# Kernel optimization log

Measured on AMD Instinct MI355X. Metric: run time of the kernel, lower is better.

The kernel has to match this reference:

```python
import jax, jax.numpy as jnp
import numpy as np

N = 256        # nagents
HID = 256      # hid_size
OBS = 128      # obs_size
GAT_HID = 128  # gat_hid_size
H1 = 4         # gat_num_heads (first processor)
H2 = 1         # gat_num_heads_out (second processor)
NACT = 10      # single action head
NEG = 0.2      # leaky relu negative slope


def _lin(k, fan_in, fan_out, s=0.05):
    kw, kb = jax.random.split(k)
    return (jax.random.normal(kw, (fan_in, fan_out), jnp.float32) * s,
            jax.random.normal(kb, (fan_out,), jnp.float32) * s)


def setup_inputs() -> dict:
    key = jax.random.key(0)
    ks = jax.random.split(key, 32)
    p = {}
    p['obs'] = jax.random.normal(ks[0], (1, N, OBS), jnp.float32)
    p['hidden_state'] = jax.random.normal(ks[1], (N, HID), jnp.float32)
    p['cell_state'] = jax.random.normal(ks[2], (N, HID), jnp.float32)
    p['w_obs'], p['b_obs'] = _lin(ks[3], OBS, HID)
    p['w_ih'], p['b_ih'] = _lin(ks[4], HID, 4 * HID)   # LSTMCell input->gates (i,f,g,o)
    p['w_hh'], p['b_hh'] = _lin(ks[5], HID, 4 * HID)
    p['w_me'], p['b_me'] = _lin(ks[6], HID, HID)        # message encoder
    p['w_md'], p['b_md'] = _lin(ks[7], HID, HID)        # message decoder
    # sub_scheduler_mlp1: 2*HID -> HID//2 -> HID//8 -> 2
    p['s1_w1'], p['s1_b1'] = _lin(ks[8], 2 * HID, HID // 2)
    p['s1_w2'], p['s1_b2'] = _lin(ks[9], HID // 2, HID // 8)
    p['s1_w3'], p['s1_b3'] = _lin(ks[10], HID // 8, 2)
    # sub_scheduler_mlp2 (learn_second_graph)
    p['s2_w1'], p['s2_b1'] = _lin(ks[11], 2 * HID, HID // 2)
    p['s2_w2'], p['s2_b2'] = _lin(ks[12], HID // 2, HID // 8)
    p['s2_w3'], p['s2_b3'] = _lin(ks[13], HID // 8, 2)
    # GAT1: HID -> H1*GAT_HID (concat heads)
    p['g1_w'] = jax.random.normal(ks[14], (HID, H1 * GAT_HID), jnp.float32) * 0.05
    p['g1_ai'] = jax.random.normal(ks[15], (H1, GAT_HID), jnp.float32) * 0.05
    p['g1_aj'] = jax.random.normal(ks[16], (H1, GAT_HID), jnp.float32) * 0.05
    p['g1_b'] = jax.random.normal(ks[17], (H1 * GAT_HID,), jnp.float32) * 0.05
    # GAT2: H1*GAT_HID -> HID (average over heads)
    p['g2_w'] = jax.random.normal(ks[18], (H1 * GAT_HID, H2 * HID), jnp.float32) * 0.05
    p['g2_ai'] = jax.random.normal(ks[19], (H2, HID), jnp.float32) * 0.05
    p['g2_aj'] = jax.random.normal(ks[20], (H2, HID), jnp.float32) * 0.05
    p['g2_b'] = jax.random.normal(ks[21], (HID,), jnp.float32) * 0.05
    p['w_v'], p['b_v'] = _lin(ks[22], 2 * HID, 1)
    p['w_a'], p['b_a'] = _lin(ks[23], 2 * HID, NACT)
    return p


def _sub_scheduler(h, w1, b1, w2, b2, w3, b3, mask, key):
    # pairwise concat: pair[i,j] = [h_i, h_j]  -> [n, n, 2*hid]
    n, d = h.shape
    pair = jnp.concatenate([jnp.broadcast_to(h[:, None, :], (n, n, d)),
                            jnp.broadcast_to(h[None, :, :], (n, n, d))], axis=-1)
    z = jax.nn.relu(pair @ w1 + b1)
    z = jax.nn.relu(z @ w2 + b2)
    logits = z @ w3 + b3                                # [n, n, 2]
    # gumbel-softmax (tau=1, hard=True, straight-through)
    u = jax.random.uniform(key, logits.shape, minval=1e-10, maxval=1.0)
    gumbel = -jnp.log(-jnp.log(u))
    y = jax.nn.softmax(logits + gumbel, axis=-1)
    y_hard = jax.nn.one_hot(jnp.argmax(y, axis=-1), 2, dtype=y.dtype)
    y = y_hard + y - jax.lax.stop_gradient(y)
    adj = y[..., 1] * mask * mask.T                     # mask [n,1]
    return adj


def _gat(x, adj, W, ai, aj, b, average):
    # dense-adjacency multi-head GAT, self_loop_type=1 (force self loops)
    n = x.shape[0]
    heads, of = ai.shape
    h = (x @ W).reshape(n, heads, of)                   # [n, heads, out]
    eye = jnp.eye(n, dtype=x.dtype)
    adj = adj * (1.0 - eye) + eye
    ci = jnp.einsum('nhf,hf->nh', h, ai)
    cj = jnp.einsum('nhf,hf->nh', h, aj)
    e = jax.nn.leaky_relu(ci[:, None, :] + cj[None, :, :], NEG)   # [n, n, heads]
    att = jnp.where(adj[:, :, None] > 0, e, jnp.float32(-9e15))
    att = jax.nn.softmax(att, axis=1)
    att = att * adj[:, :, None]
    out = jnp.einsum('ijh,jhf->ihf', att, h)            # aggregate over neighbors j
    out = out.mean(axis=1) if average else out.reshape(n, heads * of)
    return out + b


def reference(obs, hidden_state, cell_state, w_obs, b_obs, w_ih, b_ih, w_hh, b_hh,
              w_me, b_me, w_md, b_md,
              s1_w1, s1_b1, s1_w2, s1_b2, s1_w3, s1_b3,
              s2_w1, s2_b1, s2_w2, s2_b2, s2_w3, s2_b3,
              g1_w, g1_ai, g1_aj, g1_b, g2_w, g2_ai, g2_aj, g2_b,
              w_v, b_v, w_a, b_a):
    x = (obs @ w_obs + b_obs)[0]                        # [n, hid]
    # LSTMCell, torch gate order (i, f, g, o)
    gates = x @ w_ih + b_ih + hidden_state @ w_hh + b_hh
    i, f, g, o = jnp.split(gates, 4, axis=-1)
    c_new = jax.nn.sigmoid(f) * cell_state + jax.nn.sigmoid(i) * jnp.tanh(g)
    h_new = jax.nn.sigmoid(o) * jnp.tanh(c_new)
    mask = jnp.ones((N, 1), jnp.float32)                # all agents alive
    comm = (h_new @ w_me + b_me) * mask
    comm_ori = comm
    adj1 = _sub_scheduler(comm, s1_w1, s1_b1, s1_w2, s1_b2, s1_w3, s1_b3,
                          mask, jax.random.key(1))
    comm = jax.nn.elu(_gat(comm, adj1, g1_w, g1_ai, g1_aj, g1_b, average=False))
    adj2 = _sub_scheduler(comm_ori, s2_w1, s2_b1, s2_w2, s2_b2, s2_w3, s2_b3,
                          mask, jax.random.key(2))
    comm = _gat(comm, adj2, g2_w, g2_ai, g2_aj, g2_b, average=True)
    comm = (comm * mask) @ w_md + b_md
    value = jnp.concatenate([h_new, comm], axis=-1) @ w_v + b_v      # [n, 1]
    hc = jnp.concatenate([h_new.reshape(1, N, HID), comm.reshape(1, N, HID)], axis=-1)
    action_out = jax.nn.log_softmax(hc @ w_a + b_a, axis=-1)         # [1, n, nact]
    return action_out, value, h_new, c_new
```

## Files before the change

kernel.cpp:

```cpp
#include <hip/hip_runtime.h>
#include <stdint.h>
#include <math.h>

#define NA 256

typedef __attribute__((ext_vector_type(4))) float f32x4;
typedef __attribute__((ext_vector_type(8))) short bfrag;
typedef __attribute__((ext_vector_type(4))) float cfrag;

__device__ __forceinline__ uint32_t rotl32_(uint32_t v, int d) {
    return (v << d) | (v >> (32 - d));
}

__device__ uint32_t jax_random_bits(uint32_t key_lo, uint32_t flat) {
    uint32_t a, b;
    bool first;
    if (flat < 65536u) { a = flat; b = flat + 65536u; first = true; }
    else               { a = flat - 65536u; b = flat; first = false; }
    uint32_t ks0 = 0u, ks1 = key_lo, ks2 = 0u ^ key_lo ^ 0x1BD11BDAu;
    uint32_t x0 = a + ks0, x1 = b + ks1;
    const int r0[4] = {13, 15, 26, 6};
    const int r1[4] = {17, 29, 16, 24};
#define TF_R4(RS) { for (int rr = 0; rr < 4; ++rr) { x0 += x1; x1 = rotl32_(x1, RS[rr]); x1 ^= x0; } }
    TF_R4(r0); x0 += ks1; x1 += ks2 + 1u;
    TF_R4(r1); x0 += ks2; x1 += ks0 + 2u;
    TF_R4(r0); x0 += ks0; x1 += ks1 + 3u;
    TF_R4(r1); x0 += ks1; x1 += ks2 + 4u;
    TF_R4(r0); x0 += ks2; x1 += ks0 + 5u;
#undef TF_R4
    return first ? x0 : x1;
}

__device__ float jax_gumbel(uint32_t key_lo, uint32_t flat) {
    uint32_t bits = jax_random_bits(key_lo, flat);
    uint32_t v = (bits >> 9) | 0x3F800000u;
    float u = __uint_as_float(v) - 1.0f;
    u = u + 1e-10f;
    u = fmaxf(1e-10f, u);
    return -logf(-logf(u));
}

__device__ __forceinline__ uint32_t f2bf(float f) {
    uint32_t u = __float_as_uint(f);
    return (u + 0x7FFFu + ((u >> 16) & 1u)) >> 16;
}

__global__ __launch_bounds__(256) void k_lstm(
        const float* __restrict__ obs, const float* __restrict__ hs,
        const float* __restrict__ cs,
        const float* __restrict__ w_obs, const float* __restrict__ b_obs,
        const float* __restrict__ w_ih, const float* __restrict__ b_ih,
        const float* __restrict__ w_hh, const float* __restrict__ b_hh,
        float* __restrict__ h_out, float* __restrict__ c_out) {
    __shared__ float o_l[8][128];
    __shared__ float h_l[8][256];
    __shared__ float x_l[8][256];
    __shared__ float red[8192];
    int r0 = blockIdx.x * 8, c0 = blockIdx.y * 32, t = threadIdx.x;
    ((f32x4*)o_l)[t] = ((const f32x4*)(obs + r0 * 128))[t];
    ((f32x4*)h_l)[t] = ((const f32x4*)(hs + r0 * 256))[t];
    ((f32x4*)h_l)[t + 256] = ((const f32x4*)(hs + r0 * 256))[t + 256];
    __syncthreads();
    {
        int ks = t >> 6, q = t & 63;
        f32x4 acc[8];
#pragma unroll
        for (int r = 0; r < 8; ++r) acc[r] = (f32x4){0.f, 0.f, 0.f, 0.f};
#pragma unroll
        for (int k = ks * 32; k < ks * 32 + 32; ++k) {
            f32x4 w = *(const f32x4*)(w_obs + k * 256 + q * 4);
#pragma unroll
            for (int r = 0; r < 8; ++r) {
                float xv = o_l[r][k];
                acc[r].x += xv * w.x; acc[r].y += xv * w.y;
                acc[r].z += xv * w.z; acc[r].w += xv * w.w;
            }
        }
#pragma unroll
        for (int r = 0; r < 8; ++r)
            *(f32x4*)&red[(ks * 8 + r) * 256 + q * 4] = acc[r];
    }
    __syncthreads();
    {
#pragma unroll
        for (int rep = 0; rep < 8; ++rep) {
            int o = t + rep * 256;
            int r = o >> 8, c = o & 255;
            float s = b_obs[c];
#pragma unroll
            for (int k2 = 0; k2 < 4; ++k2) s += red[(k2 * 8 + r) * 256 + c];
            x_l[r][c] = s;
        }
    }
    __syncthreads();
    {
        int ks = t >> 5, cg = t & 31;
        int g = cg >> 3, qd = cg & 7;
        int col = g * 256 + c0 + qd * 4;
        const float* W = (ks < 4) ? w_ih : w_hh;
        const float* xl = (ks < 4) ? &x_l[0][0] : &h_l[0][0];
        int kb = (ks & 3) * 64;
        f32x4 acc[8];
#pragma unroll
        for (int r = 0; r < 8; ++r) acc[r] = (f32x4){0.f, 0.f, 0.f, 0.f};
#pragma unroll
        for (int kk = 0; kk < 64; ++kk) {
            int k = kb + kk;
            f32x4 w = *(const f32x4*)(W + k * 1024 + col);
#pragma unroll
            for (int r = 0; r < 8; ++r) {
                float xv = xl[r * 256 + k];
                acc[r].x += xv * w.x; acc[r].y += xv * w.y;
                acc[r].z += xv * w.z; acc[r].w += xv * w.w;
            }
        }
        __syncthreads();
#pragma unroll
        for (int r = 0; r < 8; ++r)
            *(f32x4*)&red[(ks * 8 + r) * 128 + cg * 4] = acc[r];
    }
    __syncthreads();
    {
        int r = t >> 5, hc = t & 31;
        int gc = c0 + hc;
        float gate[4];
#pragma unroll
        for (int g = 0; g < 4; ++g) {
            float s = b_ih[g * 256 + gc] + b_hh[g * 256 + gc];
#pragma unroll
            for (int ks = 0; ks < 8; ++ks) s += red[(ks * 8 + r) * 128 + g * 32 + hc];
            gate[g] = s;
        }
        float ig = 1.f / (1.f + expf(-gate[0]));
        float fg = 1.f / (1.f + expf(-gate[1]));
        float gg = tanhf(gate[2]);
        float og = 1.f / (1.f + expf(-gate[3]));
        float cn = fg * cs[(r0 + r) * 256 + gc] + ig * gg;
        float hn = og * tanhf(cn);
        h_out[(r0 + r) * 256 + gc] = hn;
        c_out[(r0 + r) * 256 + gc] = cn;
    }
}

template<int K>
__device__ __forceinline__ void gemm_core(const float* __restrict__ X, int xs, int r0,
                                          const float* __restrict__ W, int ws,
                                          const float* __restrict__ bias,
                                          float* __restrict__ Y, int ys, int t,
                                          float* xr, float* red) {
    constexpr int KQ = K / 4;
#pragma unroll
    for (int q = t; q < 2 * K; q += 256) {
        int r = q / KQ, c = q % KQ;
        ((f32x4*)xr)[r * KQ + c] = ((const f32x4*)(X + (r0 + r) * xs))[c];
    }
    __syncthreads();
    constexpr int KP = K / 16;
    int qd = t & 15, ks = t >> 4;
    f32x4 acc[8];
#pragma unroll
    for (int r = 0; r < 8; ++r) acc[r] = (f32x4){0.f, 0.f, 0.f, 0.f};
#pragma unroll
    for (int k = ks * KP; k < ks * KP + KP; ++k) {
        f32x4 w = *(const f32x4*)(W + k * ws + qd * 4);
#pragma unroll
        for (int r = 0; r < 8; ++r) {
            float xv = xr[r * K + k];
            acc[r].x += xv * w.x; acc[r].y += xv * w.y;
            acc[r].z += xv * w.z; acc[r].w += xv * w.w;
        }
    }
#pragma unroll
    for (int r = 0; r < 8; ++r)
        *(f32x4*)&red[(ks * 8 + r) * 64 + qd * 4] = acc[r];
    __syncthreads();
#pragma unroll
    for (int rep = 0; rep < 2; ++rep) {
        int o = t + rep * 256;
        int r = o >> 6, c = o & 63;
        float s = bias ? bias[c] : 0.f;
#pragma unroll
        for (int ks2 = 0; ks2 < 16; ++ks2) s += red[(ks2 * 8 + r) * 64 + c];
        Y[(r0 + r) * ys + c] = s;
    }
}

template<int K>
__global__ __launch_bounds__(256) void k_gemm(const float* __restrict__ X, int xs,
                                              const float* __restrict__ W, int ws,
                                              const float* __restrict__ bias,
                                              float* __restrict__ Y, int ys) {
    __shared__ float xr[8 * K];
    __shared__ float red[16 * 8 * 64];
    int cb = blockIdx.y * 64;
    gemm_core<K>(X, xs, blockIdx.x * 8, W + cb, ws, bias ? bias + cb : nullptr,
                 Y + cb, ys, threadIdx.x, xr, red);
}

__global__ __launch_bounds__(256) void k_mgemm(const float* __restrict__ comm,
        const float* __restrict__ g1_w,
        const float* __restrict__ s1w1, const float* __restrict__ s1b1,
        const float* __restrict__ s2w1, const float* __restrict__ s2b1,
        float* __restrict__ h1, float* __restrict__ A1, float* __restrict__ B1,
        float* __restrict__ A2, float* __restrict__ B2) {
    __shared__ float xr[8 * 256];
    __shared__ float red[16 * 8 * 64];
    int y = blockIdx.y;
    const float* W; int ws; const float* bias; float* Y; int ys;
    if (y < 8) {
        W = g1_w + y * 64; ws = 512; bias = nullptr; Y = h1 + y * 64; ys = 512;
    } else {
        int idx = y - 8;
        int sel = idx >> 2, part = (idx >> 1) & 1, half = idx & 1;
        W = (sel ? s2w1 : s1w1) + part * (256 * 128) + half * 64; ws = 128;
        bias = part ? nullptr : ((sel ? s2b1 : s1b1) + half * 64);
        float* tgt = sel ? (part ? B2 : A2) : (part ? B1 : A1);
        Y = tgt + half * 64; ys = 128;
    }
    gemm_core<256>(comm, 256, blockIdx.x * 8, W, ws, bias, Y, ys, threadIdx.x, xr, red);
}

__global__ __launch_bounds__(256) void k_sched(
        const float* __restrict__ A1, const float* __restrict__ B1,
        const float* __restrict__ s1w2, const float* __restrict__ s1b2,
        const float* __restrict__ s1w3, const float* __restrict__ s1b3,
        const float* __restrict__ A2, const float* __restrict__ B2,
        const float* __restrict__ s2w2, const float* __restrict__ s2b2,
        const float* __restrict__ s2w3, const float* __restrict__ s2b3,
        float* __restrict__ adj1, float* __restrict__ adj2) {
    __shared__ __align__(16) char z1z2[65536];
    __shared__ __align__(16) char w2l[8192];
    __shared__ float a_l[128];
    __shared__ float b2_l[32], w3_l[64], b3_l[2];
    int i = blockIdx.x, t = threadIdx.x, s = blockIdx.y;
    const float* A  = s ? A2 : A1;
    const float* B  = s ? B2 : B1;
    const float* w2 = s ? s2w2 : s1w2;
    const float* b2 = s ? s2b2 : s1b2;
    const float* w3 = s ? s2w3 : s1w3;
    const float* b3 = s ? s2b3 : s1b3;
    float* adj = s ? adj2 : adj1;
    uint32_t key_lo = (uint32_t)(s + 1);

    if (t < 32) ((f32x4*)a_l)[t] = ((const f32x4*)(A + i * 128))[t];
    if (t < 32) b2_l[t] = b2[t];
    if (t < 64) w3_l[t] = w3[t];
    if (t < 2)  b3_l[t] = b3[t];
    {
        int c = t & 31, kq = t >> 5;
        uint32_t* dst = (uint32_t*)w2l;
#pragma unroll
        for (int e = 0; e < 8; ++e) {
            int k = kq * 16 + e * 2;
            uint32_t word = f2bf(w2[k * 32 + c]) | (f2bf(w2[(k + 1) * 32 + c]) << 16);
            int byte = (c * 256 + k * 2) ^ ((c & 7) << 4);
            dst[byte >> 2] = word;
        }
    }
    __syncthreads();
#pragma unroll
    for (int rep = 0; rep < 4; ++rep) {
        int j = (t >> 2) + rep * 64;
        int kq = t & 3;
        const f32x4* bp = (const f32x4*)(B + j * 128 + kq * 32);
        uint32_t words[16];
#pragma unroll
        for (int q = 0; q < 8; ++q) {
            f32x4 bv = bp[q];
            int k = kq * 32 + q * 4;
            float z0 = fmaxf(a_l[k] + bv.x, 0.f);
            float z1v = fmaxf(a_l[k + 1] + bv.y, 0.f);
            float z2v = fmaxf(a_l[k + 2] + bv.z, 0.f);
            float z3v = fmaxf(a_l[k + 3] + bv.w, 0.f);
            words[q * 2]     = f2bf(z0) | (f2bf(z1v) << 16);
            words[q * 2 + 1] = f2bf(z2v) | (f2bf(z3v) << 16);
        }
#pragma unroll
        for (int w4 = 0; w4 < 4; ++w4) {
            int byte = (j * 256 + kq * 64 + w4 * 16) ^ ((j & 7) << 4);
            *(uint4*)(z1z2 + byte) = make_uint4(words[w4 * 4], words[w4 * 4 + 1],
                                                words[w4 * 4 + 2], words[w4 * 4 + 3]);
        }
    }
    __syncthreads();
    int w = t >> 6, l = t & 63;
    bfrag bf[2][4];
#pragma unroll
    for (int ct = 0; ct < 2; ++ct)
#pragma unroll
        for (int ks = 0; ks < 4; ++ks) {
            int col = ct * 16 + (l & 15);
            int k = ks * 32 + (l >> 4) * 8;
            int byte = (col * 256 + k * 2) ^ ((col & 7) << 4);
            bf[ct][ks] = *(bfrag*)(w2l + byte);
        }
    cfrag acc[4][2];
    cfrag zz = {0.f, 0.f, 0.f, 0.f};
#pragma unroll
    for (int rt = 0; rt < 4; ++rt) { acc[rt][0] = zz; acc[rt][1] = zz; }
#pragma unroll
    for (int rt = 0; rt < 4; ++rt) {
        int j = (w * 4 + rt) * 16 + (l & 15);
#pragma unroll
        for (int ks = 0; ks < 4; ++ks) {
            int byte = (j * 256 + (ks * 32 + (l >> 4) * 8) * 2) ^ ((j & 7) << 4);
            bfrag af = *(bfrag*)(z1z2 + byte);
            acc[rt][0] = __builtin_amdgcn_mfma_f32_16x16x32_bf16(af, bf[0][ks], acc[rt][0], 0, 0, 0);
            acc[rt][1] = __builtin_amdgcn_mfma_f32_16x16x32_bf16(af, bf[1][ks], acc[rt][1], 0, 0, 0);
        }
    }
    __syncthreads();
    float* z2 = (float*)z1z2;
#pragma unroll
    for (int rt = 0; rt < 4; ++rt)
#pragma unroll
        for (int ct = 0; ct < 2; ++ct)
#pragma unroll
            for (int r = 0; r < 4; ++r) {
                int j = (w * 4 + rt) * 16 + (l >> 4) * 4 + r;
                int c = ct * 16 + (l & 15);
                z2[j * 36 + c] = acc[rt][ct][r];
            }
    __syncthreads();
    {
        int j = t;
        float p0 = 0.f, p1 = 0.f;
#pragma unroll
        for (int c = 0; c < 32; ++c) {
            float zv = fmaxf(z2[j * 36 + c] + b2_l[c], 0.f);
            p0 += zv * w3_l[2 * c];
            p1 += zv * w3_l[2 * c + 1];
        }
        float l0 = p0 + b3_l[0], l1 = p1 + b3_l[1];
        uint32_t flat = (uint32_t)(i * 256 + j) * 2u;
        float g0 = jax_gumbel(key_lo, flat);
        float g1 = jax_gumbel(key_lo, flat + 1u);
        adj[i * 256 + j] = (l1 + g1 > l0 + g0) ? 1.0f : 0.0f;
    }
}

__global__ void k_attc(const float* __restrict__ H, const float* __restrict__ ai,
                       const float* __restrict__ aj, float* __restrict__ ci,
                       float* __restrict__ cj, int heads, int F) {
    int n = blockIdx.x, lane = threadIdx.x;
    for (int h = 0; h < heads; ++h) {
        float pi = 0.f, pj = 0.f;
        for (int f = lane; f < F; f += 64) {
            float v = H[n * heads * F + h * F + f];
            pi += v * ai[h * F + f];
            pj += v * aj[h * F + f];
        }
        for (int off = 32; off; off >>= 1) {
            pi += __shfl_xor(pi, off);
            pj += __shfl_xor(pj, off);
        }
        if (lane == 0) { ci[n * heads + h] = pi; cj[n * heads + h] = pj; }
    }
}

__global__ __launch_bounds__(256) void k_gat1(const float* __restrict__ H,
        const float* __restrict__ adj, const float* __restrict__ ci,
        const float* __restrict__ cj, const float* __restrict__ bias,
        float* __restrict__ out) {
    __shared__ float att[2][4][256];
    __shared__ float red[4][2][256];
    int i0 = blockIdx.x * 2, cb = blockIdx.y * 256, t = threadIdx.x;
#pragma unroll
    for (int r = 0; r < 2; ++r) {
        int i = i0 + r;
        float adjv = (t == i) ? 1.f : adj[i * 256 + t];
#pragma unroll
        for (int h = 0; h < 4; ++h) {
            float e = ci[i * 4 + h] + cj[t * 4 + h];
            e = e >= 0.f ? e : 0.2f * e;
            att[r][h][t] = adjv > 0.f ? e : -INFINITY;
        }
    }
    __syncthreads();
    {
        int wv = t >> 6, lane = t & 63;
        for (int p = wv; p < 8; p += 4) {
            int r = p >> 2, h = p & 3;
            float* ar = att[r][h];
            float m = -INFINITY;
            for (int j = lane; j < 256; j += 64) m = fmaxf(m, ar[j]);
            for (int off = 32; off; off >>= 1) m = fmaxf(m, __shfl_xor(m, off));
            float vals[4], sm = 0.f;
#pragma unroll
            for (int q = 0; q < 4; ++q) {
                float v = expf(ar[lane + 64 * q] - m);
                vals[q] = v; sm += v;
            }
            for (int off = 32; off; off >>= 1) sm += __shfl_xor(sm, off);
            float inv = 1.f / sm;
#pragma unroll
            for (int q = 0; q < 4; ++q) ar[lane + 64 * q] = vals[q] * inv;
        }
    }
    __syncthreads();
    {
        int q = t & 63, js = t >> 6;
        int c = cb + q * 4;
        int h = c >> 7;
        f32x4 a0 = {0.f, 0.f, 0.f, 0.f}, a1 = a0;
        const float* ar0 = att[0][h];
        const float* ar1 = att[1][h];
#pragma unroll
        for (int j = js * 64; j < js * 64 + 64; ++j) {
            f32x4 hv = *(const f32x4*)(H + j * 512 + c);
            float v0 = ar0[j], v1 = ar1[j];
            a0.x += v0 * hv.x; a0.y += v0 * hv.y; a0.z += v0 * hv.z; a0.w += v0 * hv.w;
            a1.x += v1 * hv.x; a1.y += v1 * hv.y; a1.z += v1 * hv.z; a1.w += v1 * hv.w;
        }
        *(f32x4*)&red[js][0][q * 4] = a0;
        *(f32x4*)&red[js][1][q * 4] = a1;
    }
    __syncthreads();
#pragma unroll
    for (int rep = 0; rep < 2; ++rep) {
        int o = t + rep * 256;
        int r = o >> 8, c = o & 255;
        float s = red[0][r][c] + red[1][r][c] + red[2][r][c] + red[3][r][c] + bias[cb + c];
        out[(i0 + r) * 512 + cb + c] = s > 0.f ? s : expm1f(s);
    }
}

__global__ __launch_bounds__(256) void k_final(const float* __restrict__ H,
        const float* __restrict__ adj, const float* __restrict__ ci,
        const float* __restrict__ cj, const float* __restrict__ g2_b,
        const float* __restrict__ w_md, const float* __restrict__ b_md,
        const float* __restrict__ h_new,
        const float* __restrict__ w_v, const float* __restrict__ b_v,
        const float* __restrict__ w_a, const float* __restrict__ b_a,
        float* __restrict__ value, float* __restrict__ action) {
    __shared__ float att[256];
    __shared__ float buf[4][256];
    __shared__ float out2[256];
    __shared__ float comm3[256];
    __shared__ float hrow[256];
    __shared__ float hred[4][16];
    __shared__ float vred[4];
    int i = blockIdx.x, t = threadIdx.x;
    hrow[t] = h_new[i * 256 + t];
    {
        float adjv = (t == i) ? 1.f : adj[i * 256 + t];
        float e = ci[i] + cj[t];
        e = e >= 0.f ? e : 0.2f * e;
        att[t] = adjv > 0.f ? e : -INFINITY;
    }
    __syncthreads();
    {
        int lane = t & 63;
        float m = -INFINITY;
        for (int j = lane; j < 256; j += 64) m = fmaxf(m, att[j]);
        for (int off = 32; off; off >>= 1) m = fmaxf(m, __shfl_xor(m, off));
        float sm = 0.f;
        for (int j = lane; j < 256; j += 64) sm += expf(att[j] - m);
        for (int off = 32; off; off >>= 1) sm += __shfl_xor(sm, off);
        float inv = 1.f / sm;
        float myval = expf(att[t] - m) * inv;
        __syncthreads();
        att[t] = myval;
    }
    __syncthreads();
    {
        int q = t & 63, js = t >> 6;
        f32x4 acc = {0.f, 0.f, 0.f, 0.f};
#pragma unroll
        for (int j = js * 64; j < js * 64 + 64; ++j) {
            f32x4 hv = *(const f32x4*)(H + j * 256 + q * 4);
            float av = att[j];
            acc.x += av * hv.x; acc.y += av * hv.y; acc.z += av * hv.z; acc.w += av * hv.w;
        }
        *(f32x4*)&buf[js][q * 4] = acc;
    }
    __syncthreads();
    out2[t] = buf[0][t] + buf[1][t] + buf[2][t] + buf[3][t] + g2_b[t];
    __syncthreads();
    {
        int q = t & 63, ks = t >> 6;
        f32x4 acc = {0.f, 0.f, 0.f, 0.f};
#pragma unroll
        for (int k = ks * 64; k < ks * 64 + 64; ++k) {
            f32x4 wv = *(const f32x4*)(w_md + k * 256 + q * 4);
            float xv = out2[k];
            acc.x += xv * wv.x; acc.y += xv * wv.y; acc.z += xv * wv.z; acc.w += xv * wv.w;
        }
        *(f32x4*)&buf[ks][q * 4] = acc;
    }
    __syncthreads();
    comm3[t] = buf[0][t] + buf[1][t] + buf[2][t] + buf[3][t] + b_md[t];
    __syncthreads();
    int w = t >> 6, l = t & 63;
    {
        float p = hrow[t] * w_v[t] + comm3[t] * w_v[256 + t];
        for (int off = 32; off; off >>= 1) p += __shfl_xor(p, off);
        if (l == 0) vred[w] = p;
    }
    {
        int o = l & 15;
        int kseg = w * 4 + (l >> 4);
        float acc = 0.f;
        if (o < 10) {
#pragma unroll
            for (int kk = 0; kk < 32; ++kk) {
                int k = kseg * 32 + kk;
                float x = (kseg < 8) ? hrow[k] : comm3[k - 256];
                acc += x * w_a[k * 10 + o];
            }
        }
        acc += __shfl_xor(acc, 16);
        acc += __shfl_xor(acc, 32);
        if (l < 16) hred[w][l] = acc;
    }
    __syncthreads();
    if (t < 16) {
        int o = t;
        float logit = (o < 10)
            ? hred[0][o] + hred[1][o] + hred[2][o] + hred[3][o] + b_a[o]
            : -INFINITY;
        float m = logit;
        for (int off = 8; off; off >>= 1) m = fmaxf(m, __shfl_xor(m, off));
        float ex = (o < 10) ? expf(logit - m) : 0.f;
        float sm = ex;
        for (int off = 8; off; off >>= 1) sm += __shfl_xor(sm, off);
        if (o < 10) action[i * 10 + o] = logit - m - logf(sm);
        if (o == 0) value[i] = vred[0] + vred[1] + vred[2] + vred[3] + b_v[0];
    }
}

extern "C" void kernel_launch(void* const* d_in, const int* in_sizes, int n_in,
                              void* d_out, int out_size, void* d_ws, size_t ws_size,
                              hipStream_t stream) {
    const float* obs   = (const float*)d_in[0];
    const float* hs    = (const float*)d_in[1];
    const float* cs    = (const float*)d_in[2];
    const float* w_obs = (const float*)d_in[3];
    const float* b_obs = (const float*)d_in[4];
    const float* w_ih  = (const float*)d_in[5];
    const float* b_ih  = (const float*)d_in[6];
    const float* w_hh  = (const float*)d_in[7];
    const float* b_hh  = (const float*)d_in[8];
    const float* w_me  = (const float*)d_in[9];
    const float* b_me  = (const float*)d_in[10];
    const float* w_md  = (const float*)d_in[11];
    const float* b_md  = (const float*)d_in[12];
    const float* s1_w1 = (const float*)d_in[13];
    const float* s1_b1 = (const float*)d_in[14];
    const float* s1_w2 = (const float*)d_in[15];
    const float* s1_b2 = (const float*)d_in[16];
    const float* s1_w3 = (const float*)d_in[17];
    const float* s1_b3 = (const float*)d_in[18];
    const float* s2_w1 = (const float*)d_in[19];
    const float* s2_b1 = (const float*)d_in[20];
    const float* s2_w2 = (const float*)d_in[21];
    const float* s2_b2 = (const float*)d_in[22];
    const float* s2_w3 = (const float*)d_in[23];
    const float* s2_b3 = (const float*)d_in[24];
    const float* g1_w  = (const float*)d_in[25];
    const float* g1_ai = (const float*)d_in[26];
    const float* g1_aj = (const float*)d_in[27];
    const float* g1_b  = (const float*)d_in[28];
    const float* g2_w  = (const float*)d_in[29];
    const float* g2_ai = (const float*)d_in[30];
    const float* g2_aj = (const float*)d_in[31];
    const float* g2_b  = (const float*)d_in[32];
    const float* w_v   = (const float*)d_in[33];
    const float* b_v   = (const float*)d_in[34];
    const float* w_a   = (const float*)d_in[35];
    const float* b_a   = (const float*)d_in[36];

    float* out = (float*)d_out;
    float* action = out;
    float* value  = out + 2560;
    float* h_new  = out + 2816;
    float* c_new  = out + 68352;

    float* ws = (float*)d_ws;
    float* comm  = ws;
    float* A1    = ws + 65536;
    float* B1    = ws + 98304;
    float* A2    = ws + 131072;
    float* B2    = ws + 163840;
    float* adj1  = ws + 196608;
    float* adj2  = ws + 262144;
    float* h1    = ws + 327680;
    float* ci1   = ws + 458752;
    float* cj1   = ws + 459776;
    float* comm2 = ws + 460800;
    float* h2    = ws + 591872;
    float* ci2   = ws + 657408;
    float* cj2   = ws + 657664;

    k_lstm<<<dim3(32, 8), 256, 0, stream>>>(obs, hs, cs, w_obs, b_obs,
                                            w_ih, b_ih, w_hh, b_hh, h_new, c_new);
    k_gemm<256><<<dim3(32, 4), 256, 0, stream>>>(h_new, 256, w_me, 256, b_me, comm, 256);
    k_mgemm<<<dim3(32, 16), 256, 0, stream>>>(comm, g1_w, s1_w1, s1_b1, s2_w1, s2_b1,
                                              h1, A1, B1, A2, B2);
    k_sched<<<dim3(256, 2), 256, 0, stream>>>(A1, B1, s1_w2, s1_b2, s1_w3, s1_b3,
                                              A2, B2, s2_w2, s2_b2, s2_w3, s2_b3,
                                              adj1, adj2);
    k_attc<<<NA, 64, 0, stream>>>(h1, g1_ai, g1_aj, ci1, cj1, 4, 128);
    k_gat1<<<dim3(128, 2), 256, 0, stream>>>(h1, adj1, ci1, cj1, g1_b, comm2);
    k_gemm<512><<<dim3(32, 4), 256, 0, stream>>>(comm2, 512, g2_w, 256, nullptr, h2, 256);
    k_attc<<<NA, 64, 0, stream>>>(h2, g2_ai, g2_aj, ci2, cj2, 1, 256);
    k_final<<<NA, 256, 0, stream>>>(h2, adj2, ci2, cj2, g2_b, w_md, b_md, h_new,
                                    w_v, b_v, w_a, b_a, value, action);
}
```

Baseline: 73.71 us.

## Fuse all stages into one cooperative persistent kernel with grid syncs

```diff
diff --git a/kernel.cpp b/kernel.cpp
--- a/kernel.cpp
+++ b/kernel.cpp
@@ -1,12 +1,15 @@
 #include <hip/hip_runtime.h>
+#include <hip/hip_cooperative_groups.h>
 #include <stdint.h>
 #include <math.h>
 
-#define NA 256
+namespace cg = cooperative_groups;
 
 typedef __attribute__((ext_vector_type(4))) float f32x4;
 typedef __attribute__((ext_vector_type(8))) short bfrag;
 typedef __attribute__((ext_vector_type(4))) float cfrag;
+
+#define SM_BYTES 53248
 
 __device__ __forceinline__ uint32_t rotl32_(uint32_t v, int d) {
     return (v << d) | (v >> (32 - d));
@@ -45,21 +48,27 @@
     return (u + 0x7FFFu + ((u >> 16) & 1u)) >> 16;
 }
 
-__global__ __launch_bounds__(256) void k_lstm(
-        const float* __restrict__ obs, const float* __restrict__ hs,
-        const float* __restrict__ cs,
-        const float* __restrict__ w_obs, const float* __restrict__ b_obs,
-        const float* __restrict__ w_ih, const float* __restrict__ b_ih,
-        const float* __restrict__ w_hh, const float* __restrict__ b_hh,
-        float* __restrict__ h_out, float* __restrict__ c_out) {
-    __shared__ float o_l[8][128];
-    __shared__ float h_l[8][256];
-    __shared__ float x_l[8][256];
-    __shared__ float red[8192];
-    int r0 = blockIdx.x * 8, c0 = blockIdx.y * 32, t = threadIdx.x;
-    ((f32x4*)o_l)[t] = ((const f32x4*)(obs + r0 * 128))[t];
-    ((f32x4*)h_l)[t] = ((const f32x4*)(hs + r0 * 256))[t];
-    ((f32x4*)h_l)[t + 256] = ((const f32x4*)(hs + r0 * 256))[t + 256];
+struct KParams {
+    const float *obs, *hs, *cs, *w_obs, *b_obs, *w_ih, *b_ih, *w_hh, *b_hh;
+    const float *w_me, *b_me, *w_md, *b_md;
+    const float *s1w1, *s1b1, *s1w2, *s1b2, *s1w3, *s1b3;
+    const float *s2w1, *s2b1, *s2w2, *s2b2, *s2w3, *s2b3;
+    const float *g1w, *g1ai, *g1aj, *g1b, *g2w, *g2ai, *g2aj, *g2b;
+    const float *wv, *bv, *wa, *ba;
+    float *h_new, *c_new, *value, *action;
+    float *comm, *A1, *B1, *A2, *B2, *adj1, *adj2, *h1, *ci1, *cj1;
+    float *comm2, *h2, *ci2, *cj2;
+};
+
+__device__ __forceinline__ void lstm_stage(const KParams& p, char* SM, int b, int t) {
+    float* o_l = (float*)SM;
+    float* h_l = (float*)(SM + 4096);
+    float* x_l = (float*)(SM + 12288);
+    float* red = (float*)(SM + 20480);
+    int r0 = (b & 31) * 8, c0 = (b >> 5) * 32;
+    ((f32x4*)o_l)[t] = ((const f32x4*)(p.obs + r0 * 128))[t];
+    ((f32x4*)h_l)[t] = ((const f32x4*)(p.hs + r0 * 256))[t];
+    ((f32x4*)h_l)[t + 256] = ((const f32x4*)(p.hs + r0 * 256))[t + 256];
     __syncthreads();
     {
         int ks = t >> 6, q = t & 63;
@@ -68,10 +77,10 @@
         for (int r = 0; r < 8; ++r) acc[r] = (f32x4){0.f, 0.f, 0.f, 0.f};
 #pragma unroll
         for (int k = ks * 32; k < ks * 32 + 32; ++k) {
-            f32x4 w = *(const f32x4*)(w_obs + k * 256 + q * 4);
+            f32x4 w = *(const f32x4*)(p.w_obs + k * 256 + q * 4);
 #pragma unroll
             for (int r = 0; r < 8; ++r) {
-                float xv = o_l[r][k];
+                float xv = o_l[r * 128 + k];
                 acc[r].x += xv * w.x; acc[r].y += xv * w.y;
                 acc[r].z += xv * w.z; acc[r].w += xv * w.w;
             }
@@ -81,24 +90,22 @@
             *(f32x4*)&red[(ks * 8 + r) * 256 + q * 4] = acc[r];
     }
     __syncthreads();
-    {
-#pragma unroll
-        for (int rep = 0; rep < 8; ++rep) {
-            int o = t + rep * 256;
-            int r = o >> 8, c = o & 255;
-            float s = b_obs[c];
-#pragma unroll
-            for (int k2 = 0; k2 < 4; ++k2) s += red[(k2 * 8 + r) * 256 + c];
-            x_l[r][c] = s;
-        }
-    }
-    __syncthreads();
-    {
-        int ks = t >> 5, cg = t & 31;
-        int g = cg >> 3, qd = cg & 7;
-        int col = g * 256 + c0 + qd * 4;
-        const float* W = (ks < 4) ? w_ih : w_hh;
-        const float* xl = (ks < 4) ? &x_l[0][0] : &h_l[0][0];
+#pragma unroll
+    for (int rep = 0; rep < 8; ++rep) {
+        int o = t + rep * 256;
+        int r = o >> 8, c = o & 255;
+        float s = p.b_obs[c];
+#pragma unroll
+        for (int k2 = 0; k2 < 4; ++k2) s += red[(k2 * 8 + r) * 256 + c];
+        x_l[r * 256 + c] = s;
+    }
+    __syncthreads();
+    {
+        int ks = t >> 5, cg2 = t & 31;
+        int g2 = cg2 >> 3, qd = cg2 & 7;
+        int col = g2 * 256 + c0 + qd * 4;
+        const float* W = (ks < 4) ? p.w_ih : p.w_hh;
+        const float* xl = (ks < 4) ? x_l : h_l;
         int kb = (ks & 3) * 64;
         f32x4 acc[8];
 #pragma unroll
@@ -117,7 +124,7 @@
         __syncthreads();
 #pragma unroll
         for (int r = 0; r < 8; ++r)
-            *(f32x4*)&red[(ks * 8 + r) * 128 + cg * 4] = acc[r];
+            *(f32x4*)&red[(ks * 8 + r) * 128 + cg2 * 4] = acc[r];
     }
     __syncthreads();
     {
@@ -125,26 +132,26 @@
         int gc = c0 + hc;
         float gate[4];
 #pragma unroll
-        for (int g = 0; g < 4; ++g) {
-            float s = b_ih[g * 256 + gc] + b_hh[g * 256 + gc];
-#pragma unroll
-            for (int ks = 0; ks < 8; ++ks) s += red[(ks * 8 + r) * 128 + g * 32 + hc];
-            gate[g] = s;
+        for (int g2 = 0; g2 < 4; ++g2) {
+            float s = p.b_ih[g2 * 256 + gc] + p.b_hh[g2 * 256 + gc];
+#pragma unroll
+            for (int ks = 0; ks < 8; ++ks) s += red[(ks * 8 + r) * 128 + g2 * 32 + hc];
+            gate[g2] = s;
         }
         float ig = 1.f / (1.f + expf(-gate[0]));
         float fg = 1.f / (1.f + expf(-gate[1]));
         float gg = tanhf(gate[2]);
         float og = 1.f / (1.f + expf(-gate[3]));
-        float cn = fg * cs[(r0 + r) * 256 + gc] + ig * gg;
+        float cn = fg * p.cs[(r0 + r) * 256 + gc] + ig * gg;
         float hn = og * tanhf(cn);
-        h_out[(r0 + r) * 256 + gc] = hn;
-        c_out[(r0 + r) * 256 + gc] = cn;
+        p.h_new[(r0 + r) * 256 + gc] = hn;
+        p.c_new[(r0 + r) * 256 + gc] = cn;
     }
 }
 
 template<int K>
 __device__ __forceinline__ void gemm_core(const float* __restrict__ X, int xs, int r0,
-                                          const float* __restrict__ W, int ws,
+                                          const float* __restrict__ W, int wsb,
                                           const float* __restrict__ bias,
                                           float* __restrict__ Y, int ys, int t,
                                           float* xr, float* red) {
@@ -162,7 +169,7 @@
     for (int r = 0; r < 8; ++r) acc[r] = (f32x4){0.f, 0.f, 0.f, 0.f};
 #pragma unroll
     for (int k = ks * KP; k < ks * KP + KP; ++k) {
-        f32x4 w = *(const f32x4*)(W + k * ws + qd * 4);
+        f32x4 w = *(const f32x4*)(W + k * wsb + qd * 4);
 #pragma unroll
         for (int r = 0; r < 8; ++r) {
             float xv = xr[r * K + k];
@@ -185,61 +192,52 @@
     }
 }
 
-template<int K>
-__global__ __launch_bounds__(256) void k_gemm(const float* __restrict__ X, int xs,
-                                              const float* __restrict__ W, int ws,
-                                              const float* __restrict__ bias,
-                                              float* __restrict__ Y, int ys) {
-    __shared__ float xr[8 * K];
-    __shared__ float red[16 * 8 * 64];
-    int cb = blockIdx.y * 64;
-    gemm_core<K>(X, xs, blockIdx.x * 8, W + cb, ws, bias ? bias + cb : nullptr,
-                 Y + cb, ys, threadIdx.x, xr, red);
-}
-
-__global__ __launch_bounds__(256) void k_mgemm(const float* __restrict__ comm,
-        const float* __restrict__ g1_w,
-        const float* __restrict__ s1w1, const float* __restrict__ s1b1,
-        const float* __restrict__ s2w1, const float* __restrict__ s2b1,
-        float* __restrict__ h1, float* __restrict__ A1, float* __restrict__ B1,
-        float* __restrict__ A2, float* __restrict__ B2) {
-    __shared__ float xr[8 * 256];
-    __shared__ float red[16 * 8 * 64];
-    int y = blockIdx.y;
-    const float* W; int ws; const float* bias; float* Y; int ys;
-    if (y < 8) {
-        W = g1_w + y * 64; ws = 512; bias = nullptr; Y = h1 + y * 64; ys = 512;
-    } else {
-        int idx = y - 8;
-        int sel = idx >> 2, part = (idx >> 1) & 1, half = idx & 1;
-        W = (sel ? s2w1 : s1w1) + part * (256 * 128) + half * 64; ws = 128;
-        bias = part ? nullptr : ((sel ? s2b1 : s1b1) + half * 64);
-        float* tgt = sel ? (part ? B2 : A2) : (part ? B1 : A1);
-        Y = tgt + half * 64; ys = 128;
-    }
-    gemm_core<256>(comm, 256, blockIdx.x * 8, W, ws, bias, Y, ys, threadIdx.x, xr, red);
-}
-
-__global__ __launch_bounds__(256) void k_sched(
-        const float* __restrict__ A1, const float* __restrict__ B1,
-        const float* __restrict__ s1w2, const float* __restrict__ s1b2,
-        const float* __restrict__ s1w3, const float* __restrict__ s1b3,
-        const float* __restrict__ A2, const float* __restrict__ B2,
-        const float* __restrict__ s2w2, const float* __restrict__ s2b2,
-        const float* __restrict__ s2w3, const float* __restrict__ s2b3,
-        float* __restrict__ adj1, float* __restrict__ adj2) {
-    __shared__ __align__(16) char z1z2[65536];
-    __shared__ __align__(16) char w2l[8192];
-    __shared__ float a_l[128];
-    __shared__ float b2_l[32], w3_l[64], b3_l[2];
-    int i = blockIdx.x, t = threadIdx.x, s = blockIdx.y;
-    const float* A  = s ? A2 : A1;
-    const float* B  = s ? B2 : B1;
-    const float* w2 = s ? s2w2 : s1w2;
-    const float* b2 = s ? s2b2 : s1b2;
-    const float* w3 = s ? s2w3 : s1w3;
-    const float* b3 = s ? s2b3 : s1b3;
-    float* adj = s ? adj2 : adj1;
+__device__ __forceinline__ void comm_stage(const KParams& p, char* SM, int b, int t) {
+    if (b >= 128) return;
+    float* xr = (float*)SM;
+    float* red = (float*)(SM + 16384);
+    int cb = (b >> 5) * 64;
+    gemm_core<256>(p.h_new, 256, (b & 31) * 8, p.w_me + cb, 256, p.b_me + cb,
+                   p.comm + cb, 256, t, xr, red);
+}
+
+__device__ __forceinline__ void mgemm_stage(const KParams& p, char* SM, int b, int t) {
+    float* xr = (float*)SM;
+    float* red = (float*)(SM + 16384);
+    int bx = b & 31;
+#pragma unroll
+    for (int pass = 0; pass < 2; ++pass) {
+        int y = (b >> 5) + pass * 8;
+        const float* W; int wsb; const float* bias; float* Y; int ys;
+        if (y < 8) {
+            W = p.g1w + y * 64; wsb = 512; bias = nullptr; Y = p.h1 + y * 64; ys = 512;
+        } else {
+            int idx = y - 8;
+            int sel = idx >> 2, part = (idx >> 1) & 1, half = idx & 1;
+            W = (sel ? p.s2w1 : p.s1w1) + part * (256 * 128) + half * 64; wsb = 128;
+            bias = part ? nullptr : ((sel ? p.s2b1 : p.s1b1) + half * 64);
+            float* tgt = sel ? (part ? p.B2 : p.A2) : (part ? p.B1 : p.A1);
+            Y = tgt + half * 64; ys = 128;
+        }
+        gemm_core<256>(p.comm, 256, bx * 8, W, wsb, bias, Y, ys, t, xr, red);
+        __syncthreads();
+    }
+}
+
+__device__ __forceinline__ void sched_body(const KParams& p, char* SM, int i, int s, int t) {
+    char* z1z2 = SM;
+    char* w2l  = SM + 32768;
+    float* a_l  = (float*)(SM + 40960);
+    float* b2_l = (float*)(SM + 41472);
+    float* w3_l = (float*)(SM + 41600);
+    float* b3_l = (float*)(SM + 41856);
+    const float* A  = s ? p.A2 : p.A1;
+    const float* B  = s ? p.B2 : p.B1;
+    const float* w2 = s ? p.s2w2 : p.s1w2;
+    const float* b2 = s ? p.s2b2 : p.s1b2;
+    const float* w3 = s ? p.s2w3 : p.s1w3;
+    const float* b3 = s ? p.s2b3 : p.s1b3;
+    float* adj = s ? p.adj2 : p.adj1;
     uint32_t key_lo = (uint32_t)(s + 1);
 
     if (t < 32) ((f32x4*)a_l)[t] = ((const f32x4*)(A + i * 128))[t];
@@ -258,31 +256,6 @@
         }
     }
     __syncthreads();
-#pragma unroll
-    for (int rep = 0; rep < 4; ++rep) {
-        int j = (t >> 2) + rep * 64;
-        int kq = t & 3;
-        const f32x4* bp = (const f32x4*)(B + j * 128 + kq * 32);
-        uint32_t words[16];
-#pragma unroll
-        for (int q = 0; q < 8; ++q) {
-            f32x4 bv = bp[q];
-            int k = kq * 32 + q * 4;
-            float z0 = fmaxf(a_l[k] + bv.x, 0.f);
-            float z1v = fmaxf(a_l[k + 1] + bv.y, 0.f);
-            float z2v = fmaxf(a_l[k + 2] + bv.z, 0.f);
-            float z3v = fmaxf(a_l[k + 3] + bv.w, 0.f);
-            words[q * 2]     = f2bf(z0) | (f2bf(z1v) << 16);
-            words[q * 2 + 1] = f2bf(z2v) | (f2bf(z3v) << 16);
-        }
-#pragma unroll
-        for (int w4 = 0; w4 < 4; ++w4) {
-            int byte = (j * 256 + kq * 64 + w4 * 16) ^ ((j & 7) << 4);
-            *(uint4*)(z1z2 + byte) = make_uint4(words[w4 * 4], words[w4 * 4 + 1],
-                                                words[w4 * 4 + 2], words[w4 * 4 + 3]);
-        }
-    }
-    __syncthreads();
     int w = t >> 6, l = t & 63;
     bfrag bf[2][4];
 #pragma unroll
@@ -294,94 +267,124 @@
             int byte = (col * 256 + k * 2) ^ ((col & 7) << 4);
             bf[ct][ks] = *(bfrag*)(w2l + byte);
         }
-    cfrag acc[4][2];
-    cfrag zz = {0.f, 0.f, 0.f, 0.f};
-#pragma unroll
-    for (int rt = 0; rt < 4; ++rt) { acc[rt][0] = zz; acc[rt][1] = zz; }
-#pragma unroll
-    for (int rt = 0; rt < 4; ++rt) {
-        int j = (w * 4 + rt) * 16 + (l & 15);
-#pragma unroll
-        for (int ks = 0; ks < 4; ++ks) {
-            int byte = (j * 256 + (ks * 32 + (l >> 4) * 8) * 2) ^ ((j & 7) << 4);
-            bfrag af = *(bfrag*)(z1z2 + byte);
-            acc[rt][0] = __builtin_amdgcn_mfma_f32_16x16x32_bf16(af, bf[0][ks], acc[rt][0], 0, 0, 0);
-            acc[rt][1] = __builtin_amdgcn_mfma_f32_16x16x32_bf16(af, bf[1][ks], acc[rt][1], 0, 0, 0);
-        }
-    }
-    __syncthreads();
-    float* z2 = (float*)z1z2;
-#pragma unroll
-    for (int rt = 0; rt < 4; ++rt)
-#pragma unroll
-        for (int ct = 0; ct < 2; ++ct)
-#pragma unroll
-            for (int r = 0; r < 4; ++r) {
-                int j = (w * 4 + rt) * 16 + (l >> 4) * 4 + r;
-                int c = ct * 16 + (l & 15);
-                z2[j * 36 + c] = acc[rt][ct][r];
-            }
-    __syncthreads();
-    {
-        int j = t;
-        float p0 = 0.f, p1 = 0.f;
-#pragma unroll
-        for (int c = 0; c < 32; ++c) {
-            float zv = fmaxf(z2[j * 36 + c] + b2_l[c], 0.f);
-            p0 += zv * w3_l[2 * c];
-            p1 += zv * w3_l[2 * c + 1];
-        }
-        float l0 = p0 + b3_l[0], l1 = p1 + b3_l[1];
-        uint32_t flat = (uint32_t)(i * 256 + j) * 2u;
-        float g0 = jax_gumbel(key_lo, flat);
-        float g1 = jax_gumbel(key_lo, flat + 1u);
-        adj[i * 256 + j] = (l1 + g1 > l0 + g0) ? 1.0f : 0.0f;
-    }
-}
-
-__global__ void k_attc(const float* __restrict__ H, const float* __restrict__ ai,
-                       const float* __restrict__ aj, float* __restrict__ ci,
-                       float* __restrict__ cj, int heads, int F) {
-    int n = blockIdx.x, lane = threadIdx.x;
-    for (int h = 0; h < heads; ++h) {
-        float pi = 0.f, pj = 0.f;
-        for (int f = lane; f < F; f += 64) {
-            float v = H[n * heads * F + h * F + f];
-            pi += v * ai[h * F + f];
-            pj += v * aj[h * F + f];
-        }
-        for (int off = 32; off; off >>= 1) {
-            pi += __shfl_xor(pi, off);
-            pj += __shfl_xor(pj, off);
-        }
-        if (lane == 0) { ci[n * heads + h] = pi; cj[n * heads + h] = pj; }
-    }
-}
-
-__global__ __launch_bounds__(256) void k_gat1(const float* __restrict__ H,
-        const float* __restrict__ adj, const float* __restrict__ ci,
-        const float* __restrict__ cj, const float* __restrict__ bias,
-        float* __restrict__ out) {
-    __shared__ float att[2][4][256];
-    __shared__ float red[4][2][256];
-    int i0 = blockIdx.x * 2, cb = blockIdx.y * 256, t = threadIdx.x;
+#pragma unroll
+    for (int jh = 0; jh < 2; ++jh) {
+        int jb = jh * 128;
+#pragma unroll
+        for (int rep = 0; rep < 2; ++rep) {
+            int jl = (t >> 2) + rep * 64;
+            int kq = t & 3;
+            const f32x4* bp = (const f32x4*)(B + (jb + jl) * 128 + kq * 32);
+            uint32_t words[16];
+#pragma unroll
+            for (int q = 0; q < 8; ++q) {
+                f32x4 bv = bp[q];
+                int k = kq * 32 + q * 4;
+                float z0 = fmaxf(a_l[k] + bv.x, 0.f);
+                float z1v = fmaxf(a_l[k + 1] + bv.y, 0.f);
+                float z2v = fmaxf(a_l[k + 2] + bv.z, 0.f);
+                float z3v = fmaxf(a_l[k + 3] + bv.w, 0.f);
+                words[q * 2]     = f2bf(z0) | (f2bf(z1v) << 16);
+                words[q * 2 + 1] = f2bf(z2v) | (f2bf(z3v) << 16);
+            }
+#pragma unroll
+            for (int w4 = 0; w4 < 4; ++w4) {
+                int byte = (jl * 256 + kq * 64 + w4 * 16) ^ ((jl & 7) << 4);
+                *(uint4*)(z1z2 + byte) = make_uint4(words[w4 * 4], words[w4 * 4 + 1],
+                                                    words[w4 * 4 + 2], words[w4 * 4 + 3]);
+            }
+        }
+        __syncthreads();
+        cfrag acc[2][2];
+        cfrag zz = {0.f, 0.f, 0.f, 0.f};
+#pragma unroll
+        for (int rt = 0; rt < 2; ++rt) { acc[rt][0] = zz; acc[rt][1] = zz; }
+#pragma unroll
+        for (int rt = 0; rt < 2; ++rt) {
+            int jl = (w * 2 + rt) * 16 + (l & 15);
+#pragma unroll
+            for (int ks = 0; ks < 4; ++ks) {
+                int byte = (jl * 256 + (ks * 32 + (l >> 4) * 8) * 2) ^ ((jl & 7) << 4);
+                bfrag af = *(bfrag*)(z1z2 + byte);
+                acc[rt][0] = __builtin_amdgcn_mfma_f32_16x16x32_bf16(af, bf[0][ks], acc[rt][0], 0, 0, 0);
+                acc[rt][1] = __builtin_amdgcn_mfma_f32_16x16x32_bf16(af, bf[1][ks], acc[rt][1], 0, 0, 0);
+            }
+        }
+        __syncthreads();
+        float* z2 = (float*)z1z2;
+#pragma unroll
+        for (int rt = 0; rt < 2; ++rt)
+#pragma unroll
+            for (int ct = 0; ct < 2; ++ct)
+#pragma unroll
+                for (int r = 0; r < 4; ++r) {
+                    int jl = (w * 2 + rt) * 16 + (l >> 4) * 4 + r;
+                    int c = ct * 16 + (l & 15);
+                    z2[jl * 36 + c] = acc[rt][ct][r];
+                }
+        __syncthreads();
+        if (t < 128) {
+            int j = jb + t;
+            float p0 = 0.f, p1 = 0.f;
+#pragma unroll
+            for (int c = 0; c < 32; ++c) {
+                float zv = fmaxf(z2[t * 36 + c] + b2_l[c], 0.f);
+                p0 += zv * w3_l[2 * c];
+                p1 += zv * w3_l[2 * c + 1];
+            }
+            float l0 = p0 + b3_l[0], l1 = p1 + b3_l[1];
+            uint32_t flat = (uint32_t)(i * 256 + j) * 2u;
+            float g0 = jax_gumbel(key_lo, flat);
+            float g1 = jax_gumbel(key_lo, flat + 1u);
+            adj[i * 256 + j] = (l1 + g1 > l0 + g0) ? 1.0f : 0.0f;
+        }
+        __syncthreads();
+    }
+}
+
+__device__ __forceinline__ void sched_attc_stage(const KParams& p, char* SM, int b, int t) {
+#pragma unroll
+    for (int s = 0; s < 2; ++s) {
+        __syncthreads();
+        sched_body(p, SM, b, s, t);
+    }
+    int h = t >> 6, lane = t & 63, n = b;
+    float pi = 0.f, pj = 0.f;
+#pragma unroll
+    for (int f = lane; f < 128; f += 64) {
+        float v = p.h1[n * 512 + h * 128 + f];
+        pi += v * p.g1ai[h * 128 + f];
+        pj += v * p.g1aj[h * 128 + f];
+    }
+#pragma unroll
+    for (int off = 32; off; off >>= 1) {
+        pi += __shfl_xor(pi, off);
+        pj += __shfl_xor(pj, off);
+    }
+    if (lane == 0) { p.ci1[n * 4 + h] = pi; p.cj1[n * 4 + h] = pj; }
+}
+
+__device__ __forceinline__ void gat1_stage(const KParams& p, char* SM, int b, int t) {
+    float* att = (float*)SM;
+    float* red = (float*)(SM + 8192);
+    int i0 = (b & 127) * 2, cb = (b >> 7) * 256;
 #pragma unroll
     for (int r = 0; r < 2; ++r) {
         int i = i0 + r;
-        float adjv = (t == i) ? 1.f : adj[i * 256 + t];
+        float adjv = (t == i) ? 1.f : p.adj1[i * 256 + t];
 #pragma unroll
         for (int h = 0; h < 4; ++h) {
-            float e = ci[i * 4 + h] + cj[t * 4 + h];
+            float e = p.ci1[i * 4 + h] + p.cj1[t * 4 + h];
             e = e >= 0.f ? e : 0.2f * e;
-            att[r][h][t] = adjv > 0.f ? e : -INFINITY;
+            att[(r * 4 + h) * 256 + t] = adjv > 0.f ? e : -INFINITY;
         }
     }
     __syncthreads();
     {
         int wv = t >> 6, lane = t & 63;
-        for (int p = wv; p < 8; p += 4) {
-            int r = p >> 2, h = p & 3;
-            float* ar = att[r][h];
+        for (int pp = wv; pp < 8; pp += 4) {
+            int r = pp >> 2, h = pp & 3;
+            float* ar = att + (r * 4 + h) * 256;
             float m = -INFINITY;
             for (int j = lane; j < 256; j += 64) m = fmaxf(m, ar[j]);
             for (int off = 32; off; off >>= 1) m = fmaxf(m, __shfl_xor(m, off));
@@ -403,48 +406,69 @@
         int c = cb + q * 4;
         int h = c >> 7;
         f32x4 a0 = {0.f, 0.f, 0.f, 0.f}, a1 = a0;
-        const float* ar0 = att[0][h];
-        const float* ar1 = att[1][h];
+        const float* ar0 = att + (0 * 4 + h) * 256;
+        const float* ar1 = att + (1 * 4 + h) * 256;
 #pragma unroll
         for (int j = js * 64; j < js * 64 + 64; ++j) {
-            f32x4 hv = *(const f32x4*)(H + j * 512 + c);
+            f32x4 hv = *(const f32x4*)(p.h1 + j * 512 + c);
             float v0 = ar0[j], v1 = ar1[j];
             a0.x += v0 * hv.x; a0.y += v0 * hv.y; a0.z += v0 * hv.z; a0.w += v0 * hv.w;
             a1.x += v1 * hv.x; a1.y += v1 * hv.y; a1.z += v1 * hv.z; a1.w += v1 * hv.w;
         }
-        *(f32x4*)&red[js][0][q * 4] = a0;
-        *(f32x4*)&red[js][1][q * 4] = a1;
+        *(f32x4*)&red[(js * 2 + 0) * 256 + q * 4] = a0;
+        *(f32x4*)&red[(js * 2 + 1) * 256 + q * 4] = a1;
     }
     __syncthreads();
 #pragma unroll
     for (int rep = 0; rep < 2; ++rep) {
         int o = t + rep * 256;
         int r = o >> 8, c = o & 255;
-        float s = red[0][r][c] + red[1][r][c] + red[2][r][c] + red[3][r][c] + bias[cb + c];
-        out[(i0 + r) * 512 + cb + c] = s > 0.f ? s : expm1f(s);
-    }
-}
-
-__global__ __launch_bounds__(256) void k_final(const float* __restrict__ H,
-        const float* __restrict__ adj, const float* __restrict__ ci,
-        const float* __restrict__ cj, const float* __restrict__ g2_b,
-        const float* __restrict__ w_md, const float* __restrict__ b_md,
-        const float* __restrict__ h_new,
-        const float* __restrict__ w_v, const float* __restrict__ b_v,
-        const float* __restrict__ w_a, const float* __restrict__ b_a,
-        float* __restrict__ value, float* __restrict__ action) {
-    __shared__ float att[256];
-    __shared__ float buf[4][256];
-    __shared__ float out2[256];
-    __shared__ float comm3[256];
-    __shared__ float hrow[256];
-    __shared__ float hred[4][16];
-    __shared__ float vred[4];
-    int i = blockIdx.x, t = threadIdx.x;
-    hrow[t] = h_new[i * 256 + t];
-    {
-        float adjv = (t == i) ? 1.f : adj[i * 256 + t];
-        float e = ci[i] + cj[t];
+        float s = red[(0 * 2 + r) * 256 + c] + red[(1 * 2 + r) * 256 + c]
+                + red[(2 * 2 + r) * 256 + c] + red[(3 * 2 + r) * 256 + c] + p.g1b[cb + c];
+        p.comm2[(i0 + r) * 512 + cb + c] = s > 0.f ? s : expm1f(s);
+    }
+}
+
+__device__ __forceinline__ void gemm512_stage(const KParams& p, char* SM, int b, int t) {
+    if (b >= 128) return;
+    float* xr = (float*)SM;
+    float* red = (float*)(SM + 16384);
+    int cb = (b >> 5) * 64;
+    gemm_core<512>(p.comm2, 512, (b & 31) * 8, p.g2w + cb, 256, nullptr,
+                   p.h2 + cb, 256, t, xr, red);
+}
+
+__device__ __forceinline__ void attc2_stage(const KParams& p, int b, int t) {
+    int w = t >> 6, lane = t & 63, n = b;
+    if (w != 0) return;
+    float pi = 0.f, pj = 0.f;
+#pragma unroll
+    for (int f = lane; f < 256; f += 64) {
+        float v = p.h2[n * 256 + f];
+        pi += v * p.g2ai[f];
+        pj += v * p.g2aj[f];
+    }
+#pragma unroll
+    for (int off = 32; off; off >>= 1) {
+        pi += __shfl_xor(pi, off);
+        pj += __shfl_xor(pj, off);
+    }
+    if (lane == 0) { p.ci2[n] = pi; p.cj2[n] = pj; }
+}
+
+__device__ __forceinline__ void final_stage(const KParams& p, char* SM, int b, int t) {
+    float* att   = (float*)SM;
+    float* buf   = (float*)(SM + 1024);
+    float* out2  = (float*)(SM + 5120);
+    float* comm3 = (float*)(SM + 6144);
+    float* hrow  = (float*)(SM + 7168);
+    float* hred  = (float*)(SM + 8192);
+    float* vred  = (float*)(SM + 8448);
+    int i = b;
+    hrow[t] = p.h_new[i * 256 + t];
+    {
+        float adjv = (t == i) ? 1.f : p.adj2[i * 256 + t];
+        float e = p.ci2[i] + p.cj2[t];
         e = e >= 0.f ? e : 0.2f * e;
         att[t] = adjv > 0.f ? e : -INFINITY;
     }
@@ -468,34 +492,34 @@
         f32x4 acc = {0.f, 0.f, 0.f, 0.f};
 #pragma unroll
         for (int j = js * 64; j < js * 64 + 64; ++j) {
-            f32x4 hv = *(const f32x4*)(H + j * 256 + q * 4);
+            f32x4 hv = *(const f32x4*)(p.h2 + j * 256 + q * 4);
             float av = att[j];
             acc.x += av * hv.x; acc.y += av * hv.y; acc.z += av * hv.z; acc.w += av * hv.w;
         }
-        *(f32x4*)&buf[js][q * 4] = acc;
-    }
-    __syncthreads();
-    out2[t] = buf[0][t] + buf[1][t] + buf[2][t] + buf[3][t] + g2_b[t];
+        *(f32x4*)&buf[js * 256 + q * 4] = acc;
+    }
+    __syncthreads();
+    out2[t] = buf[t] + buf[256 + t] + buf[512 + t] + buf[768 + t] + p.g2b[t];
     __syncthreads();
     {
         int q = t & 63, ks = t >> 6;
         f32x4 acc = {0.f, 0.f, 0.f, 0.f};
 #pragma unroll
         for (int k = ks * 64; k < ks * 64 + 64; ++k) {
-            f32x4 wv = *(const f32x4*)(w_md + k * 256 + q * 4);
+            f32x4 wv = *(const f32x4*)(p.w_md + k * 256 + q * 4);
             float xv = out2[k];
             acc.x += xv * wv.x; acc.y += xv * wv.y; acc.z += xv * wv.z; acc.w += xv * wv.w;
         }
-        *(f32x4*)&buf[ks][q * 4] = acc;
-    }
-    __syncthreads();
-    comm3[t] = buf[0][t] + buf[1][t] + buf[2][t] + buf[3][t] + b_md[t];
+        *(f32x4*)&buf[ks * 256 + q * 4] = acc;
+    }
+    __syncthreads();
+    comm3[t] = buf[t] + buf[256 + t] + buf[512 + t] + buf[768 + t] + p.b_md[t];
     __syncthreads();
     int w = t >> 6, l = t & 63;
     {
-        float p = hrow[t] * w_v[t] + comm3[t] * w_v[256 + t];
-        for (int off = 32; off; off >>= 1) p += __shfl_xor(p, off);
-        if (l == 0) vred[w] = p;
+        float pv = hrow[t] * p.wv[t] + comm3[t] * p.wv[256 + t];
+        for (int off = 32; off; off >>= 1) pv += __shfl_xor(pv, off);
+        if (l == 0) vred[w] = pv;
     }
     {
         int o = l & 15;
@@ -506,104 +530,151 @@
             for (int kk = 0; kk < 32; ++kk) {
                 int k = kseg * 32 + kk;
                 float x = (kseg < 8) ? hrow[k] : comm3[k - 256];
-                acc += x * w_a[k * 10 + o];
+                acc += x * p.wa[k * 10 + o];
             }
         }
         acc += __shfl_xor(acc, 16);
         acc += __shfl_xor(acc, 32);
-        if (l < 16) hred[w][l] = acc;
+        if (l < 16) hred[w * 16 + l] = acc;
     }
     __syncthreads();
     if (t < 16) {
         int o = t;
         float logit = (o < 10)
-            ? hred[0][o] + hred[1][o] + hred[2][o] + hred[3][o] + b_a[o]
+            ? hred[o] + hred[16 + o] + hred[32 + o] + hred[48 + o] + p.ba[o]
             : -INFINITY;
         float m = logit;
         for (int off = 8; off; off >>= 1) m = fmaxf(m, __shfl_xor(m, off));
         float ex = (o < 10) ? expf(logit - m) : 0.f;
         float sm = ex;
         for (int off = 8; off; off >>= 1) sm += __shfl_xor(sm, off);
-        if (o < 10) action[i * 10 + o] = logit - m - logf(sm);
-        if (o == 0) value[i] = vred[0] + vred[1] + vred[2] + vred[3] + b_v[0];
-    }
+        if (o < 10) p.action[i * 10 + o] = logit - m - logf(sm);
+        if (o == 0) p.value[i] = vred[0] + vred[1] + vred[2] + vred[3] + p.bv[0];
+    }
+}
+
+__global__ __launch_bounds__(256) void k_all(KParams p) {
+    __shared__ __align__(16) char SM[SM_BYTES];
+    cg::grid_group grid = cg::this_grid();
+    int b = blockIdx.x, t = threadIdx.x;
+    lstm_stage(p, SM, b, t);        grid.sync();
+    comm_stage(p, SM, b, t);        grid.sync();
+    mgemm_stage(p, SM, b, t);       grid.sync();
+    sched_attc_stage(p, SM, b, t);  grid.sync();
+    gat1_stage(p, SM, b, t);        grid.sync();
+    gemm512_stage(p, SM, b, t);     grid.sync();
+    attc2_stage(p, b, t);           grid.sync();
+    final_stage(p, SM, b, t);
+}
+
+__global__ __launch_bounds__(256) void ks_lstm(KParams p) {
+    __shared__ __align__(16) char SM[SM_BYTES];
+    lstm_stage(p, SM, blockIdx.x, threadIdx.x);
+}
+__global__ __launch_bounds__(256) void ks_comm(KParams p) {
+    __shared__ __align__(16) char SM[SM_BYTES];
+    comm_stage(p, SM, blockIdx.x, threadIdx.x);
+}
+__global__ __launch_bounds__(256) void ks_mgemm(KParams p) {
+    __shared__ __align__(16) char SM[SM_BYTES];
+    mgemm_stage(p, SM, blockIdx.x, threadIdx.x);
+}
+__global__ __launch_bounds__(256) void ks_schedattc(KParams p) {
+    __shared__ __align__(16) char SM[SM_BYTES];
+    sched_attc_stage(p, SM, blockIdx.x, threadIdx.x);
+}
+__global__ __launch_bounds__(256) void ks_gat1(KParams p) {
+    __shared__ __align__(16) char SM[SM_BYTES];
+    gat1_stage(p, SM, blockIdx.x, threadIdx.x);
+}
+__global__ __launch_bounds__(256) void ks_gemm512(KParams p) {
+    __shared__ __align__(16) char SM[SM_BYTES];
+    gemm512_stage(p, SM, blockIdx.x, threadIdx.x);
+}
+__global__ __launch_bounds__(64) void ks_attc2(KParams p) {
+    attc2_stage(p, blockIdx.x, threadIdx.x);
+}
+__global__ __launch_bounds__(256) void ks_final(KParams p) {
+    __shared__ __align__(16) char SM[SM_BYTES];
+    final_stage(p, SM, blockIdx.x, threadIdx.x);
 }
 
 extern "C" void kernel_launch(void* const* d_in, const int* in_sizes, int n_in,
                               void* d_out, int out_size, void* d_ws, size_t ws_size,
                               hipStream_t stream) {
-    const float* obs   = (const float*)d_in[0];
-    const float* hs    = (const float*)d_in[1];
-    const float* cs    = (const float*)d_in[2];
-    const float* w_obs = (const float*)d_in[3];
-    const float* b_obs = (const float*)d_in[4];
-    const float* w_ih  = (const float*)d_in[5];
-    const float* b_ih  = (const float*)d_in[6];
-    const float* w_hh  = (const float*)d_in[7];
-    const float* b_hh  = (const float*)d_in[8];
-    const float* w_me  = (const float*)d_in[9];
-    const float* b_me  = (const float*)d_in[10];
-    const float* w_md  = (const float*)d_in[11];
-    const float* b_md  = (const float*)d_in[12];
-    const float* s1_w1 = (const float*)d_in[13];
-    const float* s1_b1 = (const float*)d_in[14];
-    const float* s1_w2 = (const float*)d_in[15];
-    const float* s1_b2 = (const float*)d_in[16];
-    const float* s1_w3 = (const float*)d_in[17];
-    const float* s1_b3 = (const float*)d_in[18];
-    const float* s2_w1 = (const float*)d_in[19];
-    const float* s2_b1 = (const float*)d_in[20];
-    const float* s2_w2 = (const float*)d_in[21];
-    const float* s2_b2 = (const float*)d_in[22];
-    const float* s2_w3 = (const float*)d_in[23];
-    const float* s2_b3 = (const float*)d_in[24];
-    const float* g1_w  = (const float*)d_in[25];
-    const float* g1_ai = (const float*)d_in[26];
-    const float* g1_aj = (const float*)d_in[27];
-    const float* g1_b  = (const float*)d_in[28];
-    const float* g2_w  = (const float*)d_in[29];
-    const float* g2_ai = (const float*)d_in[30];
-    const float* g2_aj = (const float*)d_in[31];
-    const float* g2_b  = (const float*)d_in[32];
-    const float* w_v   = (const float*)d_in[33];
-    const float* b_v   = (const float*)d_in[34];
-    const float* w_a   = (const float*)d_in[35];
-    const float* b_a   = (const float*)d_in[36];
-
     float* out = (float*)d_out;
-    float* action = out;
-    float* value  = out + 2560;
-    float* h_new  = out + 2816;
-    float* c_new  = out + 68352;
-
     float* ws = (float*)d_ws;
-    float* comm  = ws;
-    float* A1    = ws + 65536;
-    float* B1    = ws + 98304;
-    float* A2    = ws + 131072;
-    float* B2    = ws + 163840;
-    float* adj1  = ws + 196608;
-    float* adj2  = ws + 262144;
-    float* h1    = ws + 327680;
-    float* ci1   = ws + 458752;
-    float* cj1   = ws + 459776;
-    float* comm2 = ws + 460800;
-    float* h2    = ws + 591872;
-    float* ci2   = ws + 657408;
-    float* cj2   = ws + 657664;
-
-    k_lstm<<<dim3(32, 8), 256, 0, stream>>>(obs, hs, cs, w_obs, b_obs,
-                                            w_ih, b_ih, w_hh, b_hh, h_new, c_new);
-    k_gemm<256><<<dim3(32, 4), 256, 0, stream>>>(h_new, 256, w_me, 256, b_me, comm, 256);
-    k_mgemm<<<dim3(32, 16), 256, 0, stream>>>(comm, g1_w, s1_w1, s1_b1, s2_w1, s2_b1,
-                                              h1, A1, B1, A2, B2);
-    k_sched<<<dim3(256, 2), 256, 0, stream>>>(A1, B1, s1_w2, s1_b2, s1_w3, s1_b3,
-                                              A2, B2, s2_w2, s2_b2, s2_w3, s2_b3,
-                                              adj1, adj2);
-    k_attc<<<NA, 64, 0, stream>>>(h1, g1_ai, g1_aj, ci1, cj1, 4, 128);
-    k_gat1<<<dim3(128, 2), 256, 0, stream>>>(h1, adj1, ci1, cj1, g1_b, comm2);
-    k_gemm<512><<<dim3(32, 4), 256, 0, stream>>>(comm2, 512, g2_w, 256, nullptr, h2, 256);
-    k_attc<<<NA, 64, 0, stream>>>(h2, g2_ai, g2_aj, ci2, cj2, 1, 256);
-    k_final<<<NA, 256, 0, stream>>>(h2, adj2, ci2, cj2, g2_b, w_md, b_md, h_new,
-                                    w_v, b_v, w_a, b_a, value, action);
-}
+
+    KParams p;
+    p.obs   = (const float*)d_in[0];
+    p.hs    = (const float*)d_in[1];
+    p.cs    = (const float*)d_in[2];
+    p.w_obs = (const float*)d_in[3];
+    p.b_obs = (const float*)d_in[4];
+    p.w_ih  = (const float*)d_in[5];
+    p.b_ih  = (const float*)d_in[6];
+    p.w_hh  = (const float*)d_in[7];
+    p.b_hh  = (const float*)d_in[8];
+    p.w_me  = (const float*)d_in[9];
+    p.b_me  = (const float*)d_in[10];
+    p.w_md  = (const float*)d_in[11];
+    p.b_md  = (const float*)d_in[12];
+    p.s1w1  = (const float*)d_in[13];
+    p.s1b1  = (const float*)d_in[14];
+    p.s1w2  = (const float*)d_in[15];
+    p.s1b2  = (const float*)d_in[16];
+    p.s1w3  = (const float*)d_in[17];
+    p.s1b3  = (const float*)d_in[18];
+    p.s2w1  = (const float*)d_in[19];
+    p.s2b1  = (const float*)d_in[20];
+    p.s2w2  = (const float*)d_in[21];
+    p.s2b2  = (const float*)d_in[22];
+    p.s2w3  = (const float*)d_in[23];
+    p.s2b3  = (const float*)d_in[24];
+    p.g1w   = (const float*)d_in[25];
+    p.g1ai  = (const float*)d_in[26];
+    p.g1aj  = (const float*)d_in[27];
+    p.g1b   = (const float*)d_in[28];
+    p.g2w   = (const float*)d_in[29];
+    p.g2ai  = (const float*)d_in[30];
+    p.g2aj  = (const float*)d_in[31];
+    p.g2b   = (const float*)d_in[32];
+    p.wv    = (const float*)d_in[33];
+    p.bv    = (const float*)d_in[34];
+    p.wa    = (const float*)d_in[35];
+    p.ba    = (const float*)d_in[36];
+
+    p.action = out;
+    p.value  = out + 2560;
+    p.h_new  = out + 2816;
+    p.c_new  = out + 68352;
+
+    p.comm  = ws;
+    p.A1    = ws + 65536;
+    p.B1    = ws + 98304;
+    p.A2    = ws + 131072;
+    p.B2    = ws + 163840;
+    p.adj1  = ws + 196608;
+    p.adj2  = ws + 262144;
+    p.h1    = ws + 327680;
+    p.ci1   = ws + 458752;
+    p.cj1   = ws + 459776;
+    p.comm2 = ws + 460800;
+    p.h2    = ws + 591872;
+    p.ci2   = ws + 657408;
+    p.cj2   = ws + 657664;
+
+    void* args[] = { (void*)&p };
+    hipError_t err = hipLaunchCooperativeKernel((const void*)k_all, dim3(256), dim3(256),
+                                                args, 0, stream);
+    if (err != hipSuccess) {
+        ks_lstm<<<256, 256, 0, stream>>>(p);
+        ks_comm<<<128, 256, 0, stream>>>(p);
+        ks_mgemm<<<256, 256, 0, stream>>>(p);
+        ks_schedattc<<<256, 256, 0, stream>>>(p);
+        ks_gat1<<<256, 256, 0, stream>>>(p);
+        ks_gemm512<<<128, 256, 0, stream>>>(p);
+        ks_attc2<<<256, 64, 0, stream>>>(p);
+        ks_final<<<256, 256, 0, stream>>>(p);
+    }
+}
```

Result: slower. 264.9 us (+259.4%).
